# Optimization experiments

Hardware: AMD Instinct MI355X
Metric: run time of the kernel (lower is better)

The kernel has to match this reference:

```python
import jax, jax.numpy as jnp
import numpy as np
import math

S, B, D, H = 2048, 2, 1024, 16
HD = D // H  # head_dim = 64


def setup_inputs() -> dict:
    key = jax.random.key(0)
    ks = jax.random.split(key, 8)
    scale = 0.02
    return {
        "query": jax.random.normal(ks[0], (S, B, D), jnp.float32),
        "key": jax.random.normal(ks[1], (S, B, D), jnp.float32),
        "value": jax.random.normal(ks[2], (S, B, D), jnp.float32),
        "mask": jax.random.randint(ks[3], (1, S, 1, 1), 0, 2, jnp.int32),
        "w_q": jax.random.normal(ks[4], (D, D), jnp.float32) * scale,
        "b_q": jnp.zeros((D,), jnp.float32),
        "w_k": jax.random.normal(ks[5], (D, D), jnp.float32) * scale,
        "b_k": jnp.zeros((D,), jnp.float32),
        "w_v": jax.random.normal(ks[6], (D, D), jnp.float32) * scale,
        "b_v": jnp.zeros((D,), jnp.float32),
    }


def reference(query, key, value, mask, w_q, b_q, w_k, b_k, w_v, b_v):
    # Linear projections (torch Linear: x @ W^T + b); inputs are (S, B, D)
    q = query @ w_q.T + b_q
    k = key @ w_k.T + b_k
    v = value @ w_v.T + b_v
    # split heads: (S, B, H, HD)
    q = q.reshape(S, B, H, HD)
    k = k.reshape(S, B, H, HD)
    v = v.reshape(S, B, H, HD)
    # scores over (query_i, key_j, batch, head)
    scores = jnp.einsum("ibhd,jbhd->ijbh", q, k) * (1.0 / math.sqrt(HD))
    # mask (1, S, 1, 1) broadcasts against (i, j, b, h); 0 => masked
    scores = jnp.where(mask == 0, -jnp.inf, scores)
    # softmax over key axis j (original: nn.Softmax(dim=1))
    attn = jax.nn.softmax(scores, axis=1)
    out = jnp.einsum("ijbh,jbhd->ibhd", attn, v)  # (S, B, H, HD)
    return out.reshape(S, B, D)
```

## Files before the change

### kernel.cpp

```cpp
#include <hip/hip_runtime.h>
#include <stdint.h>


#define S_ 2048
#define B_ 2
#define D_ 1024
#define H_ 16
#define HD_ 64
#define M_ (S_ * B_)

typedef __bf16 bf16;
typedef bf16 bf16x8 __attribute__((ext_vector_type(8)));
typedef float floatx4 __attribute__((ext_vector_type(4)));

#define QSCALE 0.18033688011112042f

__device__ __forceinline__ void async_cp16(const bf16* g, bf16* l) {
    __builtin_amdgcn_global_load_lds(
        (const __attribute__((address_space(1))) void*)g,
        (__attribute__((address_space(3))) void*)l, 16, 0, 0);
}

__global__ __launch_bounds__(256) void mask_scan(const int* __restrict__ mask,
                                                 int* __restrict__ sidx,
                                                 int* __restrict__ cnt)
{
    __shared__ int sums[256];
    const int tid = threadIdx.x;
    int v[8], s = 0;
    #pragma unroll
    for (int j = 0; j < 8; j++) { v[j] = mask[tid * 8 + j] ? 1 : 0; s += v[j]; }
    sums[tid] = s;
    __syncthreads();
    for (int off = 1; off < 256; off <<= 1) {
        int t = (tid >= off) ? sums[tid - off] : 0;
        __syncthreads();
        sums[tid] += t;
        __syncthreads();
    }
    int base = (tid > 0) ? sums[tid - 1] : 0;
    #pragma unroll
    for (int j = 0; j < 8; j++)
        if (v[j]) { sidx[base] = tid * 8 + j; base++; }
    if (tid == 255) cnt[0] = sums[255];
}

__global__ __launch_bounds__(256) void cvt_gather(
    const float* __restrict__ xq, const float* __restrict__ xk, const float* __restrict__ xv,
    const int* __restrict__ sidx, const int* __restrict__ cnt,
    bf16* __restrict__ oq, bf16* __restrict__ ok, bf16* __restrict__ ov)
{
    const int z = blockIdx.y;
    const float* src = (z == 0) ? xq : (z == 1) ? xk : xv;
    bf16*        dst = (z == 0) ? oq : (z == 1) ? ok : ov;

    const int tid = threadIdx.x;
    const int rm  = blockIdx.x * 2 + (tid >> 7);
    int srow = rm;
    if (z != 0) {
        const int cs = rm >> 1, b = rm & 1;
        if (cs >= cnt[0]) return;
        srow = sidx[cs] * 2 + b;
    }
    const int col = (tid & 127) * 8;
    const floatx4* sp = (const floatx4*)(src + (size_t)srow * D_ + col);
    floatx4 x0 = sp[0], x1 = sp[1];
    bf16x8 v;
    #pragma unroll
    for (int j = 0; j < 4; j++) { v[j] = (bf16)x0[j]; v[4 + j] = (bf16)x1[j]; }
    *(bf16x8*)(dst + (size_t)rm * D_ + col) = v;
}

__global__ __launch_bounds__(256) void cvt3(
    const float* __restrict__ a, const float* __restrict__ b, const float* __restrict__ c,
    bf16* __restrict__ oa, bf16* __restrict__ ob, bf16* __restrict__ oc)
{
    const int z = blockIdx.z;
    const float* src = (z == 0) ? a : (z == 1) ? b : c;
    bf16*        dst = (z == 0) ? oa : (z == 1) ? ob : oc;
    const size_t i = ((size_t)blockIdx.x * 256 + threadIdx.x) * 8;
    floatx4 x0 = *(const floatx4*)(src + i);
    floatx4 x1 = *(const floatx4*)(src + i + 4);
    bf16x8 v;
    #pragma unroll
    for (int j = 0; j < 4; j++) { v[j] = (bf16)x0[j]; v[4 + j] = (bf16)x1[j]; }
    *(bf16x8*)(dst + i) = v;
}

#define TM 128
#define TN 128
#define BK 32

__global__ __launch_bounds__(256) void qkv_gemm_async(
    const bf16* __restrict__ xq, const bf16* __restrict__ xk, const bf16* __restrict__ xv,
    const bf16* __restrict__ wq, const bf16* __restrict__ wk, const bf16* __restrict__ wv,
    const float* __restrict__ bq, const float* __restrict__ bk, const float* __restrict__ bv,
    const int* __restrict__ cnt,
    bf16* __restrict__ oq, bf16* __restrict__ ok, bf16* __restrict__ ov)
{
    __shared__ __align__(16) bf16 a_lds[2][TM * BK];
    __shared__ __align__(16) bf16 b_lds[2][TN * BK];

    const int z = blockIdx.y;
    const bf16*  X  = (z == 0) ? xq : (z == 1) ? xk : xv;
    const bf16*  W  = (z == 0) ? wq : (z == 1) ? wk : wv;
    const float* Bi = (z == 0) ? bq : (z == 1) ? bk : bv;
    bf16*        O  = (z == 0) ? oq : (z == 1) ? ok : ov;

    const int f   = blockIdx.x;
    const int xcd = f & 7, t = f >> 3;
    const int m0  = ((t & 3) * 8 + xcd) * TM;
    const int n0  = (t >> 2) * TN;

    const int rows_active = (z == 0) ? M_ : 2 * cnt[0];
    if (m0 >= rows_active) return;

    const int tid  = threadIdx.x;
    const int wid  = tid >> 6;
    const int lane = tid & 63;
    const int wm = wid >> 1, wn = wid & 1;
    const int lm = lane & 15, lq = lane >> 4;

    const int a_base = ((z == 2) ? wn : wm) * 64;
    const int b_base = ((z == 2) ? wm : wn) * 64;

    floatx4 acc[4][4] = {};

    #define GEMM_STAGE(buf, kt)                                                 \
        {                                                                       \
            _Pragma("unroll")                                                   \
            for (int tt = 0; tt < 2; tt++) {                                    \
                const int cb  = (tt * 4 + wid) * 64;                            \
                const int c   = cb + lane;                                      \
                const int row = c >> 2;                                         \
                const int kcs = (c & 3) ^ ((c >> 3) & 3);                       \
                async_cp16(X + (size_t)(m0 + row) * D_ + (kt) + kcs * 8,        \
                           a_lds[buf] + cb * 8);                                \
                async_cp16(W + (size_t)(n0 + row) * D_ + (kt) + kcs * 8,        \
                           b_lds[buf] + cb * 8);                                \
            }                                                                   \
        }

    #define GEMM_DRAIN_BARRIER()                                                \
        {                                                                       \
            asm volatile("s_waitcnt vmcnt(0)" ::: "memory");                    \
            __builtin_amdgcn_sched_barrier(0);                                  \
            __syncthreads();                                                    \
        }

    GEMM_STAGE(0, 0);
    GEMM_DRAIN_BARRIER();

    const int nk = D_ / BK;
    for (int ki = 0; ki < nk; ki++) {
        const int cur = ki & 1;
        if (ki + 1 < nk) GEMM_STAGE(cur ^ 1, (ki + 1) * BK);

        const bf16* src_a = (z == 2) ? b_lds[cur] : a_lds[cur];
        const bf16* src_b = (z == 2) ? a_lds[cur] : b_lds[cur];

        bf16x8 af[4], bfv[4];
        #pragma unroll
        for (int i = 0; i < 4; i++) {
            const int r = a_base + i * 16 + lm;
            af[i] = *(const bf16x8*)(src_a + r * BK + ((lq ^ ((r >> 1) & 3)) * 8));
        }
        #pragma unroll
        for (int j = 0; j < 4; j++) {
            const int r = b_base + j * 16 + lm;
            bfv[j] = *(const bf16x8*)(src_b + r * BK + ((lq ^ ((r >> 1) & 3)) * 8));
        }
        __builtin_amdgcn_s_setprio(1);
        #pragma unroll
        for (int i = 0; i < 4; i++)
            #pragma unroll
            for (int j = 0; j < 4; j++)
                acc[i][j] = __builtin_amdgcn_mfma_f32_16x16x32_bf16(
                    af[i], bfv[j], acc[i][j], 0, 0, 0);
        __builtin_amdgcn_s_setprio(0);

        GEMM_DRAIN_BARRIER();
    }
    #undef GEMM_STAGE
    #undef GEMM_DRAIN_BARRIER

    if (z != 2) {
        #pragma unroll
        for (int j = 0; j < 4; j++) {
            const int n = n0 + wn * 64 + j * 16 + lm;
            const float bias = Bi[n];
            const int h = n >> 6, hd = n & 63;
            #pragma unroll
            for (int i = 0; i < 4; i++) {
                const int mb = m0 + wm * 64 + i * 16 + lq * 4;
                #pragma unroll
                for (int r = 0; r < 4; r++) {
                    const int m = mb + r;
                    const int row = m >> 1, b = m & 1;
                    float v = acc[i][j][r] + bias;
                    if (z == 0) v *= QSCALE;
                    O[(((size_t)(b * H_ + h)) * S_ + row) * HD_ + hd] = (bf16)v;
                }
            }
        }
    } else {
        #pragma unroll
        for (int j = 0; j < 4; j++) {
            const int m = m0 + wm * 64 + j * 16 + lm;
            const int cs = m >> 1, b = m & 1;
            #pragma unroll
            for (int i = 0; i < 4; i++) {
                const int wb = n0 + wn * 64 + i * 16 + lq * 4;
                #pragma unroll
                for (int r = 0; r < 4; r++) {
                    const int n = wb + r;
                    const float bias = Bi[n];
                    const int h = n >> 6, d = n & 63;
                    O[(((size_t)(b * H_ + h)) * HD_ + d) * S_ + cs] =
                        (bf16)(acc[i][j][r] + bias);
                }
            }
        }
    }
}

#define KT 64
#define QB 128

__global__ __launch_bounds__(256) void attn_kernel(
    const bf16* __restrict__ qw, const bf16* __restrict__ kw, const bf16* __restrict__ vtw,
    const int* __restrict__ cnt, float* __restrict__ out)
{
    __shared__ __align__(16) bf16 k_lds[2 * KT * HD_];
    __shared__ __align__(16) bf16 v_ldsT[2 * HD_ * KT];
    __shared__ __align__(16) bf16 p_lds[4 * 2 * 16 * 72];

    const int tid  = threadIdx.x;
    const int wid  = tid >> 6;
    const int lane = tid & 63;
    const int lm = lane & 15, lq = lane >> 4;
    const int bh = blockIdx.y;
    const int q0 = blockIdx.x * QB;
    const int count = cnt[0];

    const bf16* Qb  = qw  + (size_t)bh * S_ * HD_;
    const bf16* Kb  = kw  + (size_t)bh * S_ * HD_;
    const bf16* VTb = vtw + (size_t)bh * HD_ * S_;

    bf16x8 qf[2][2];
    #pragma unroll
    for (int t = 0; t < 2; t++) {
        const bf16* qp = Qb + (size_t)(q0 + wid * 32 + t * 16 + lm) * HD_;
        qf[t][0] = *(const bf16x8*)(qp + lq * 8);
        qf[t][1] = *(const bf16x8*)(qp + 32 + lq * 8);
    }

    float lsum[2][4] = {};
    floatx4 oacc[2][4] = {};
    bf16* pwb = p_lds + wid * (2 * 16 * 72);

    const int c0row = tid >> 3, c0ch = tid & 7;
    const int c1row = (tid + 256) >> 3, c1ch = tid & 7;

    {
        bf16x8 kv0 = *(const bf16x8*)(Kb + (size_t)c0row * HD_ + c0ch * 8);
        bf16x8 kv1 = *(const bf16x8*)(Kb + (size_t)c1row * HD_ + c1ch * 8);
        bf16x8 vv0 = *(const bf16x8*)(VTb + (size_t)c0row * S_ + c0ch * 8);
        bf16x8 vv1 = *(const bf16x8*)(VTb + (size_t)c1row * S_ + c1ch * 8);
        *(bf16x8*)(k_lds + c0row * 64 + ((c0ch ^ (c0row & 7)) * 8)) = kv0;
        *(bf16x8*)(k_lds + c1row * 64 + ((c1ch ^ (c1row & 7)) * 8)) = kv1;
        *(bf16x8*)(v_ldsT + c0row * 64 + ((c0ch ^ (c0row & 7)) * 8)) = vv0;
        *(bf16x8*)(v_ldsT + c1row * 64 + ((c1ch ^ (c1row & 7)) * 8)) = vv1;
    }
    __syncthreads();

    const int nt = (count + KT - 1) / KT;
    for (int it = 0; it < nt; ++it) {
        const int j0  = it * KT;
        const int cur = it & 1, nxt = cur ^ 1;
        const bool has_next = (it + 1 < nt);
        const bf16* kc = k_lds + cur * (KT * 64);
        const bf16* vc = v_ldsT + cur * (KT * 64);

        bf16x8 kreg0, kreg1, vreg0, vreg1;
        if (has_next) {
            const int jn = j0 + KT;
            kreg0 = *(const bf16x8*)(Kb + (size_t)(jn + c0row) * HD_ + c0ch * 8);
            kreg1 = *(const bf16x8*)(Kb + (size_t)(jn + c1row) * HD_ + c1ch * 8);
            vreg0 = *(const bf16x8*)(VTb + (size_t)c0row * S_ + jn + c0ch * 8);
            vreg1 = *(const bf16x8*)(VTb + (size_t)c1row * S_ + jn + c1ch * 8);
        }

        floatx4 sacc[2][4] = {};
        __builtin_amdgcn_s_setprio(1);
        #pragma unroll
        for (int ks = 0; ks < 2; ks++)
            #pragma unroll
            for (int n = 0; n < 4; n++) {
                bf16x8 kf = *(const bf16x8*)(kc + (n * 16 + lm) * 64 +
                                             (((ks * 4 + lq) ^ (lm & 7)) * 8));
                sacc[0][n] = __builtin_amdgcn_mfma_f32_16x16x32_bf16(qf[0][ks], kf, sacc[0][n], 0, 0, 0);
                sacc[1][n] = __builtin_amdgcn_mfma_f32_16x16x32_bf16(qf[1][ks], kf, sacc[1][n], 0, 0, 0);
            }
        __builtin_amdgcn_s_setprio(0);

        bool valid[4];
        #pragma unroll
        for (int n = 0; n < 4; n++)
            valid[n] = (j0 + n * 16 + lm < count);

        #pragma unroll
        for (int t = 0; t < 2; t++)
            #pragma unroll
            for (int r = 0; r < 4; r++)
                #pragma unroll
                for (int n = 0; n < 4; n++) {
                    const float p = valid[n] ? exp2f(sacc[t][n][r]) : 0.0f;
                    lsum[t][r] += p;
                    pwb[t * (16 * 72) + (lq * 4 + r) * 72 + n * 16 + lm] = (bf16)p;
                }

        asm volatile("s_waitcnt lgkmcnt(0)" ::: "memory");
        __builtin_amdgcn_sched_barrier(0);

        __builtin_amdgcn_s_setprio(1);
        #pragma unroll
        for (int ks = 0; ks < 2; ks++) {
            bf16x8 pf0 = *(const bf16x8*)(pwb + lm * 72 + ks * 32 + lq * 8);
            bf16x8 pf1 = *(const bf16x8*)(pwb + (16 * 72) + lm * 72 + ks * 32 + lq * 8);
            #pragma unroll
            for (int n = 0; n < 4; n++) {
                bf16x8 vf = *(const bf16x8*)(vc + (n * 16 + lm) * 64 +
                                             (((ks * 4 + lq) ^ (lm & 7)) * 8));
                oacc[0][n] = __builtin_amdgcn_mfma_f32_16x16x32_bf16(pf0, vf, oacc[0][n], 0, 0, 0);
                oacc[1][n] = __builtin_amdgcn_mfma_f32_16x16x32_bf16(pf1, vf, oacc[1][n], 0, 0, 0);
            }
        }
        __builtin_amdgcn_s_setprio(0);

        if (has_next) {
            bf16* kd = k_lds + nxt * (KT * 64);
            bf16* vd = v_ldsT + nxt * (KT * 64);
            *(bf16x8*)(kd + c0row * 64 + ((c0ch ^ (c0row & 7)) * 8)) = kreg0;
            *(bf16x8*)(kd + c1row * 64 + ((c1ch ^ (c1row & 7)) * 8)) = kreg1;
            *(bf16x8*)(vd + c0row * 64 + ((c0ch ^ (c0row & 7)) * 8)) = vreg0;
            *(bf16x8*)(vd + c1row * 64 + ((c1ch ^ (c1row & 7)) * 8)) = vreg1;
        }
        __syncthreads();
    }

    float invl[2][4];
    #pragma unroll
    for (int t = 0; t < 2; t++)
        #pragma unroll
        for (int r = 0; r < 4; r++) {
            float lr = lsum[t][r];
            lr += __shfl_xor(lr, 1);
            lr += __shfl_xor(lr, 2);
            lr += __shfl_xor(lr, 4);
            lr += __shfl_xor(lr, 8);
            invl[t][r] = 1.0f / lr;
        }
    const int b = bh >> 4, h = bh & 15;
    #pragma unroll
    for (int t = 0; t < 2; t++)
        #pragma unroll
        for (int n = 0; n < 4; n++)
            #pragma unroll
            for (int r = 0; r < 4; r++) {
                const int q = q0 + wid * 32 + t * 16 + lq * 4 + r;
                out[((size_t)q * B_ + b) * D_ + h * 64 + n * 16 + lm] =
                    oacc[t][n][r] * invl[t][r];
            }
}

extern "C" void kernel_launch(void* const* d_in, const int* in_sizes, int n_in,
                              void* d_out, int out_size, void* d_ws, size_t ws_size,
                              hipStream_t stream) {
    const float* xq = (const float*)d_in[0];
    const float* xk = (const float*)d_in[1];
    const float* xv = (const float*)d_in[2];
    const int*  mask = (const int*)d_in[3];
    const float* wq = (const float*)d_in[4];
    const float* bq = (const float*)d_in[5];
    const float* wk = (const float*)d_in[6];
    const float* bk = (const float*)d_in[7];
    const float* wv = (const float*)d_in[8];
    const float* bv = (const float*)d_in[9];

    const size_t NX = (size_t)M_ * D_;
    const size_t NW = (size_t)D_ * D_;
    char* ws = (char*)d_ws;
    int* cnt  = (int*)ws;
    int* sidx = cnt + 16;
    char* base = ws + 16384;

    bf16* xqb = (bf16*)base;
    bf16* xkb = xqb + NX;
    bf16* xvb = xkb + NX;
    bf16* wqb = xvb + NX;
    bf16* wkb = wqb + NW;
    bf16* wvb = wkb + NW;
    bf16* q_ws  = wvb + NW;
    bf16* k_ws  = q_ws + NX;
    bf16* vt_ws = k_ws + NX;

    mask_scan<<<1, 256, 0, stream>>>(mask, sidx, cnt);
    cvt_gather<<<dim3(M_ / 2, 3), 256, 0, stream>>>(xq, xk, xv, sidx, cnt,
                                                    xqb, xkb, xvb);
    cvt3<<<dim3(NW / 2048, 1, 3), 256, 0, stream>>>(wq, wk, wv, wqb, wkb, wvb);

    qkv_gemm_async<<<dim3(256, 3), 256, 0, stream>>>(xqb, xkb, xvb, wqb, wkb, wvb,
                                                     bq, bk, bv, cnt,
                                                     q_ws, k_ws, vt_ws);

    attn_kernel<<<dim3(S_ / QB, B_ * H_), 256, 0, stream>>>(q_ws, k_ws, vt_ws,
                                                            cnt, (float*)d_out);
}
```

Measured before the change: 219.2 us.

## Deepen GEMM async-copy pipeline with partial vmcnt waits and precomputed addresses

The projection GEMM main loop now issues loads two K-tiles ahead and waits with a partial vmcnt(4), so only the current tile's copies must finish before the barrier instead of draining all outstanding loads each iteration. After the LDS fragments are read into registers, a second barrier lets the next prefetch overwrite the buffer just consumed, so the copy overlaps with the MFMA block. Global source pointers and LDS offsets are precomputed outside the loop to cut per-stage address arithmetic. This adds one more barrier per iteration and depends on the exact count of outstanding async copies for correctness.

Result: faster. 205.4 us (-6.3%).

```diff
diff --git a/kernel.cpp b/kernel.cpp
--- a/kernel.cpp
+++ b/kernel.cpp
@@ -124,37 +124,40 @@
     const int a_base = ((z == 2) ? wn : wm) * 64;
     const int b_base = ((z == 2) ? wm : wn) * 64;
 
+    const int c0 = wid * 64 + lane;
+    const int c1 = (4 + wid) * 64 + lane;
+    const int r0 = c0 >> 2, r1 = c1 >> 2;
+    const int k0 = ((c0 & 3) ^ ((c0 >> 3) & 3)) * 8;
+    const int k1 = ((c1 & 3) ^ ((c1 >> 3) & 3)) * 8;
+    const bf16* xs0 = X + (size_t)(m0 + r0) * D_ + k0;
+    const bf16* xs1 = X + (size_t)(m0 + r1) * D_ + k1;
+    const bf16* ws0 = W + (size_t)(n0 + r0) * D_ + k0;
+    const bf16* ws1 = W + (size_t)(n0 + r1) * D_ + k1;
+    const int la0 = (wid)     * 512;
+    const int la1 = (4 + wid) * 512;
+
+    #define GEMM_STAGE(buf, kt)                                   \
+        {                                                         \
+            async_cp16(xs0 + (kt), &a_lds[buf][la0]);             \
+            async_cp16(ws0 + (kt), &b_lds[buf][la0]);             \
+            async_cp16(xs1 + (kt), &a_lds[buf][la1]);             \
+            async_cp16(ws1 + (kt), &b_lds[buf][la1]);             \
+        }
+
     floatx4 acc[4][4] = {};
 
-    #define GEMM_STAGE(buf, kt)                                                 \
-        {                                                                       \
-            _Pragma("unroll")                                                   \
-            for (int tt = 0; tt < 2; tt++) {                                    \
-                const int cb  = (tt * 4 + wid) * 64;                            \
-                const int c   = cb + lane;                                      \
-                const int row = c >> 2;                                         \
-                const int kcs = (c & 3) ^ ((c >> 3) & 3);                       \
-                async_cp16(X + (size_t)(m0 + row) * D_ + (kt) + kcs * 8,        \
-                           a_lds[buf] + cb * 8);                                \
-                async_cp16(W + (size_t)(n0 + row) * D_ + (kt) + kcs * 8,        \
-                           b_lds[buf] + cb * 8);                                \
-            }                                                                   \
-        }
-
-    #define GEMM_DRAIN_BARRIER()                                                \
-        {                                                                       \
-            asm volatile("s_waitcnt vmcnt(0)" ::: "memory");                    \
-            __builtin_amdgcn_sched_barrier(0);                                  \
-            __syncthreads();                                                    \
-        }
-
     GEMM_STAGE(0, 0);
-    GEMM_DRAIN_BARRIER();
+    GEMM_STAGE(1, BK);
 
     const int nk = D_ / BK;
     for (int ki = 0; ki < nk; ki++) {
         const int cur = ki & 1;
-        if (ki + 1 < nk) GEMM_STAGE(cur ^ 1, (ki + 1) * BK);
+
+        if (ki + 1 < nk) asm volatile("s_waitcnt vmcnt(4)" ::: "memory");
+        else             asm volatile("s_waitcnt vmcnt(0)" ::: "memory");
+        __builtin_amdgcn_sched_barrier(0);
+        __builtin_amdgcn_s_barrier();
+        __builtin_amdgcn_sched_barrier(0);
 
         const bf16* src_a = (z == 2) ? b_lds[cur] : a_lds[cur];
         const bf16* src_b = (z == 2) ? a_lds[cur] : b_lds[cur];
@@ -170,6 +173,13 @@
             const int r = b_base + j * 16 + lm;
             bfv[j] = *(const bf16x8*)(src_b + r * BK + ((lq ^ ((r >> 1) & 3)) * 8));
         }
+        asm volatile("s_waitcnt lgkmcnt(0)" ::: "memory");
+        __builtin_amdgcn_sched_barrier(0);
+        __builtin_amdgcn_s_barrier();
+        __builtin_amdgcn_sched_barrier(0);
+
+        if (ki + 2 < nk) GEMM_STAGE(cur, (ki + 2) * BK);
+
         __builtin_amdgcn_s_setprio(1);
         #pragma unroll
         for (int i = 0; i < 4; i++)
@@ -178,11 +188,8 @@
                 acc[i][j] = __builtin_amdgcn_mfma_f32_16x16x32_bf16(
                     af[i], bfv[j], acc[i][j], 0, 0, 0);
         __builtin_amdgcn_s_setprio(0);
-
-        GEMM_DRAIN_BARRIER();
     }
     #undef GEMM_STAGE
-    #undef GEMM_DRAIN_BARRIER
 
     if (z != 2) {
         #pragma unroll
```
